# Performance work log

Hardware: AMD Instinct MI355X
Metric: run time of the kernel (lower is better)

The kernel has to match this reference:

```python
import jax, jax.numpy as jnp
import numpy as np

BN_EPS = 1e-5
K = 3  # number of nearest neighbors for interpolation


def setup_inputs() -> dict:
    key = jax.random.key(0)
    ks = jax.random.split(key, 16)
    B, N1, N2 = 8, 8192, 2048
    C2, C1, H = 256, 128, 256  # in_channels, skip_channels, out_channels
    total_in = C2 + C1
    inp = {
        "xyz1": jax.random.normal(ks[0], (B, 3, N1), dtype=jnp.float32),
        "xyz2": jax.random.normal(ks[1], (B, 3, N2), dtype=jnp.float32),
        "features1": jax.random.normal(ks[2], (B, C1, N1), dtype=jnp.float32),
        "features2": jax.random.normal(ks[3], (B, C2, N2), dtype=jnp.float32),
        # SharedMLP([total_in, H, H]): two 1x1 Conv1d + BatchNorm1d (eval mode) + ReLU
        "w1": jax.random.normal(ks[4], (H, total_in), dtype=jnp.float32) * 0.05,
        "b1": jax.random.normal(ks[5], (H,), dtype=jnp.float32) * 0.01,
        "g1": 1.0 + 0.1 * jax.random.normal(ks[6], (H,), dtype=jnp.float32),
        "be1": 0.1 * jax.random.normal(ks[7], (H,), dtype=jnp.float32),
        "m1": 0.1 * jax.random.normal(ks[8], (H,), dtype=jnp.float32),
        "v1": 0.5 + jax.random.uniform(ks[9], (H,), dtype=jnp.float32),
        "w2": jax.random.normal(ks[10], (H, H), dtype=jnp.float32) * 0.05,
        "b2": jax.random.normal(ks[11], (H,), dtype=jnp.float32) * 0.01,
        "g2": 1.0 + 0.1 * jax.random.normal(ks[12], (H,), dtype=jnp.float32),
        "be2": 0.1 * jax.random.normal(ks[13], (H,), dtype=jnp.float32),
        "m2": 0.1 * jax.random.normal(ks[14], (H,), dtype=jnp.float32),
        "v2": 0.5 + jax.random.uniform(ks[15], (H,), dtype=jnp.float32),
    }
    return inp


def _conv_bn_relu(x, w, b, g, be, m, v):
    # x: [B, Cin, N], w: [Cout, Cin] (1x1 conv), BN in eval mode
    y = jnp.einsum("oc,bcn->bon", w, x) + b[None, :, None]
    y = (y - m[None, :, None]) * (g / jnp.sqrt(v + BN_EPS))[None, :, None] + be[None, :, None]
    return jax.nn.relu(y)


def reference(xyz1, xyz2, features1, features2,
              w1, b1, g1, be1, m1, v1,
              w2, b2, g2, be2, m2, v2):
    # --- squared pairwise distances [B, N1, N2] ---
    x1 = jnp.transpose(xyz1, (0, 2, 1))  # [B, N1, 3]
    x2 = jnp.transpose(xyz2, (0, 2, 1))  # [B, N2, 3]
    sq = (jnp.sum(x1 * x1, axis=-1, keepdims=True)
          + jnp.sum(x2 * x2, axis=-1)[:, None, :]
          - 2.0 * jnp.einsum("bnd,bmd->bnm", x1, x2))
    # --- k=3 nearest neighbors (smallest sq distances) ---
    neg_d, idx = jax.lax.top_k(-sq, K)          # [B, N1, K]
    dist = jnp.maximum(-neg_d, 1e-10)
    weight = 1.0 / dist
    weight = weight / jnp.sum(weight, axis=-1, keepdims=True)  # [B, N1, K]
    # --- gather neighbor features and inverse-distance interpolate ---
    feat2_t = jnp.transpose(features2, (0, 2, 1))              # [B, N2, C2]
    neighbor = jax.vmap(lambda f, i: f[i])(feat2_t, idx)       # [B, N1, K, C2]
    interp = jnp.einsum("bnkc,bnk->bnc", neighbor, weight)     # [B, N1, C2]
    interp = jnp.transpose(interp, (0, 2, 1))                  # [B, C2, N1]
    # --- concat skip features and shared MLP ---
    x = jnp.concatenate([interp, features1], axis=1)           # [B, C2+C1, N1]
    x = _conv_bn_relu(x, w1, b1, g1, be1, m1, v1)
    x = _conv_bn_relu(x, w2, b2, g2, be2, m2, v2)
    return x
```

## Files before the change

### kernel.cpp

```cpp
#include <hip/hip_runtime.h>
#include <hip/hip_bf16.h>

typedef unsigned short u16;
typedef __attribute__((ext_vector_type(4))) float f32x4;
typedef __attribute__((ext_vector_type(8))) short short8;

#define BN_EPS 1e-5f

__device__ __forceinline__ u16 f2b(float x) {
  union { float f; unsigned int u; } v; v.f = x;
  unsigned int r = (v.u + 0x7FFFu + ((v.u >> 16) & 1u)) >> 16;
  return (u16)r;
}
__device__ __forceinline__ float b2f(u16 u) {
  union { unsigned int u; float f; } v; v.u = ((unsigned int)u) << 16;
  return v.f;
}

__global__ void prep_kernel(const float* __restrict__ w1, const float* __restrict__ b1,
                            const float* __restrict__ g1, const float* __restrict__ be1,
                            const float* __restrict__ m1, const float* __restrict__ v1,
                            const float* __restrict__ w2, const float* __restrict__ b2,
                            const float* __restrict__ g2, const float* __restrict__ be2,
                            const float* __restrict__ m2, const float* __restrict__ v2,
                            u16* __restrict__ w1b, u16* __restrict__ w2b,
                            float* __restrict__ al1, float* __restrict__ bt1,
                            float* __restrict__ al2, float* __restrict__ bt2) {
  int t = threadIdx.x;
  int blk = blockIdx.x;
  if (blk < 384) {
    int id = blk * 256 + t;
    unsigned o = (unsigned)id / 384u;
    unsigned c = (unsigned)id % 384u;
    w1b[(c >> 5) * 8192 + o * 32 + (c & 31)] = f2b(w1[id]);
  } else if (blk < 640) {
    int j = (blk - 384) * 256 + t;
    unsigned o = (unsigned)j >> 8;
    unsigned c = (unsigned)j & 255u;
    w2b[(c >> 5) * 8192 + o * 32 + (c & 31)] = f2b(w2[j]);
  } else if (blk == 640) {
    float a = g1[t] / sqrtf(v1[t] + BN_EPS);
    al1[t] = a;
    bt1[t] = (b1[t] - m1[t]) * a + be1[t];
  } else {
    float a = g2[t] / sqrtf(v2[t] + BN_EPS);
    al2[t] = a;
    bt2[t] = (b2[t] - m2[t]) * a + be2[t];
  }
}

__global__ void transpose_f2_kernel(const float* __restrict__ f2, u16* __restrict__ f2t) {
  __shared__ float tile[32][33];
  int t = threadIdx.x;
  int tx = t & 31, ty = t >> 5;
  int b = blockIdx.z;
  int n2t = blockIdx.x * 32, ct = blockIdx.y * 32;
#pragma unroll
  for (int i = 0; i < 4; ++i) {
    int c = ct + ty + i * 8;
    tile[ty + i * 8][tx] = f2[((size_t)b * 256 + c) * 2048 + n2t + tx];
  }
  __syncthreads();
#pragma unroll
  for (int i = 0; i < 4; ++i) {
    int n2 = n2t + ty + i * 8;
    f2t[((size_t)b * 2048 + n2) * 256 + ct + tx] = f2b(tile[tx][ty + i * 8]);
  }
}

__global__ __launch_bounds__(256) void knn_interp_kernel(
    const float* __restrict__ xyz1, const float* __restrict__ xyz2,
    const float* __restrict__ f1, const u16* __restrict__ f2t,
    u16* __restrict__ xb) {
  union Lds {
    struct { float4 pts[2048]; float md[256 * 3]; int mi[256 * 3]; } a;
    float f1t[128 * 65];
  };
  __shared__ Lds lds;
  __shared__ float wts[64 * 3];
  __shared__ int idxs[64 * 3];

  int t = threadIdx.x;
  int b = blockIdx.x >> 7;
  int n1_0 = (blockIdx.x & 127) * 64;
  int panel = blockIdx.x;

  const float* x2 = xyz2 + b * 3 * 2048;
  for (int j = t; j < 2048; j += 256) {
    float cx = x2[j], cy = x2[2048 + j], cz = x2[4096 + j];
    float nsq = (cx * cx + cy * cy) + cz * cz;
    lds.a.pts[j] = make_float4(cx, cy, cz, nsq);
  }
  __syncthreads();

  {
    int p = t & 63, s = t >> 6;
    int n1 = n1_0 + p;
    const float* x1 = xyz1 + b * 3 * 8192;
    float bx = x1[n1], by = x1[8192 + n1], bz = x1[16384 + n1];
    float n1sq = (bx * bx + by * by) + bz * bz;
    float nx = -2.f * bx, ny = -2.f * by, nz = -2.f * bz;
    float d0 = 3.4e38f, d1 = 3.4e38f, d2 = 3.4e38f;
    int i0 = 0, i1 = 0, i2 = 0;
    int jb = s * 512;
#pragma unroll 4
    for (int jj = 0; jj < 512; ++jj) {
      float4 c = lds.a.pts[jb + jj];
      float sq = fmaf(nx, c.x, fmaf(ny, c.y, fmaf(nz, c.z, n1sq + c.w)));
      int j = jb + jj;
      bool c0 = sq < d0, c1 = sq < d1, c2 = sq < d2;
      d2 = c1 ? d1 : (c2 ? sq : d2);  i2 = c1 ? i1 : (c2 ? j : i2);
      d1 = c0 ? d0 : (c1 ? sq : d1); i1 = c0 ? i0 : (c1 ? j : i1);
      d0 = c0 ? sq : d0;             i0 = c0 ? j : i0;
    }
    lds.a.md[t * 3 + 0] = d0; lds.a.md[t * 3 + 1] = d1; lds.a.md[t * 3 + 2] = d2;
    lds.a.mi[t * 3 + 0] = i0; lds.a.mi[t * 3 + 1] = i1; lds.a.mi[t * 3 + 2] = i2;
  }
  __syncthreads();
  if (t < 64) {
    float d0 = 3.4e38f, d1 = 3.4e38f, d2 = 3.4e38f;
    int i0 = 0, i1 = 0, i2 = 0;
#pragma unroll
    for (int s = 0; s < 4; ++s) {
#pragma unroll
      for (int k = 0; k < 3; ++k) {
        float d = lds.a.md[(s * 64 + t) * 3 + k];
        int i = lds.a.mi[(s * 64 + t) * 3 + k];
        bool c0 = d < d0, c1 = d < d1, c2 = d < d2;
        i2 = c1 ? i1 : (c2 ? i : i2);
        i1 = c0 ? i0 : (c1 ? i : i1);
        i0 = c0 ? i : i0;
        d2 = c1 ? d1 : (c2 ? d : d2);
        d1 = c0 ? d0 : (c1 ? d : d1);
        d0 = c0 ? d : d0;
      }
    }
    float e0 = fmaxf(d0, 1e-10f), e1 = fmaxf(d1, 1e-10f), e2 = fmaxf(d2, 1e-10f);
    float w0 = 1.0f / e0, w1 = 1.0f / e1, w2 = 1.0f / e2;
    float sm = (w0 + w1) + w2;
    wts[t * 3 + 0] = w0 / sm; wts[t * 3 + 1] = w1 / sm; wts[t * 3 + 2] = w2 / sm;
    idxs[t * 3 + 0] = i0 * 256; idxs[t * 3 + 1] = i1 * 256; idxs[t * 3 + 2] = i2 * 256;
  }
  __syncthreads();

  {
    const u16* f2tb = f2t + (size_t)b * 2048 * 256;
    size_t xbase = (size_t)panel * 24576 + (size_t)((t >> 5) * 2048) + (t & 31);
#pragma unroll 4
    for (int p = 0; p < 64; ++p) {
      int j0 = idxs[p * 3 + 0], j1 = idxs[p * 3 + 1], j2 = idxs[p * 3 + 2];
      float w0 = wts[p * 3 + 0], w1 = wts[p * 3 + 1], w2 = wts[p * 3 + 2];
      float v = (w0 * b2f(f2tb[j0 + t]) + w1 * b2f(f2tb[j1 + t]))
                + w2 * b2f(f2tb[j2 + t]);
      xb[xbase + p * 32] = f2b(v);
    }
  }
  __syncthreads();

  {
    const float* f1b = f1 + (size_t)b * 128 * 8192 + n1_0;
    for (int it = 0; it < 32; ++it) {
      int c = it * 4 + (t >> 6);
      int n = t & 63;
      lds.f1t[c * 65 + n] = f1b[(size_t)c * 8192 + n];
    }
    __syncthreads();
    for (int it = 0; it < 32; ++it) {
      int v = it * 256 + t;
      int c = v & 127, p = v >> 7;
      float val = lds.f1t[c * 65 + p];
      xb[(size_t)panel * 24576 + (size_t)(8 + (c >> 5)) * 2048 + p * 32 + (c & 31)] = f2b(val);
    }
  }
}

__global__ __launch_bounds__(256) void gemm_fused_kernel(
    const u16* __restrict__ xin, const u16* __restrict__ w1b,
    const u16* __restrict__ w2b,
    const float* __restrict__ al1, const float* __restrict__ bt1,
    const float* __restrict__ al2, const float* __restrict__ bt2,
    float* __restrict__ fout) {
  __shared__ u16 y1t[8 * 64 * 40];
  int t = threadIdx.x;
  int panel = blockIdx.x;
  int w = t >> 6, lane = t & 63, l15 = lane & 15, quad = lane >> 4;

  f32x4 acc[4][4];
#pragma unroll
  for (int m = 0; m < 4; ++m)
#pragma unroll
    for (int n = 0; n < 4; ++n)
      acc[m][n] = (f32x4){0.f, 0.f, 0.f, 0.f};

  {
    const u16* aw = w1b + (size_t)(w * 64 + l15) * 32 + quad * 8;
    const u16* bx = xin + (size_t)panel * (12 * 2048) + (size_t)l15 * 32 + quad * 8;
    short8 af[2][4], bf[2][4];
#pragma unroll
    for (int m = 0; m < 4; ++m)
      af[0][m] = *(const short8*)(aw + m * 512);
#pragma unroll
    for (int n = 0; n < 4; ++n)
      bf[0][n] = *(const short8*)(bx + n * 512);
#pragma unroll
    for (int kt = 0; kt < 12; ++kt) {
      int cur = kt & 1, nxt = cur ^ 1;
      if (kt < 11) {
#pragma unroll
        for (int m = 0; m < 4; ++m)
          af[nxt][m] = *(const short8*)(aw + (kt + 1) * 8192 + m * 512);
#pragma unroll
        for (int n = 0; n < 4; ++n)
          bf[nxt][n] = *(const short8*)(bx + (kt + 1) * 2048 + n * 512);
      }
#pragma unroll
      for (int m = 0; m < 4; ++m)
#pragma unroll
        for (int n = 0; n < 4; ++n)
          acc[m][n] = __builtin_amdgcn_mfma_f32_16x16x32_bf16(af[cur][m], bf[cur][n], acc[m][n], 0, 0, 0);
    }
  }

  {
    float al[4][4], bt[4][4];
#pragma unroll
    for (int m = 0; m < 4; ++m)
#pragma unroll
      for (int r = 0; r < 4; ++r) {
        int o = w * 64 + m * 16 + quad * 4 + r;
        al[m][r] = al1[o];
        bt[m][r] = bt1[o];
      }
#pragma unroll
    for (int m = 0; m < 4; ++m) {
      int kt2 = w * 2 + (m >> 1);
      int osub = (m & 1) * 16 + quad * 4;
#pragma unroll
      for (int n = 0; n < 4; ++n) {
        int col = n * 16 + l15;
        ushort4 pk;
        pk.x = f2b(fmaxf(fmaf(al[m][0], acc[m][n][0], bt[m][0]), 0.f));
        pk.y = f2b(fmaxf(fmaf(al[m][1], acc[m][n][1], bt[m][1]), 0.f));
        pk.z = f2b(fmaxf(fmaf(al[m][2], acc[m][n][2], bt[m][2]), 0.f));
        pk.w = f2b(fmaxf(fmaf(al[m][3], acc[m][n][3], bt[m][3]), 0.f));
        *(ushort4*)&y1t[(kt2 * 64 + col) * 40 + osub] = pk;
      }
    }
  }
  __syncthreads();

#pragma unroll
  for (int m = 0; m < 4; ++m)
#pragma unroll
    for (int n = 0; n < 4; ++n)
      acc[m][n] = (f32x4){0.f, 0.f, 0.f, 0.f};
  {
    const u16* aw = w2b + (size_t)(w * 64 + l15) * 32 + quad * 8;
    short8 af[2][4];
#pragma unroll
    for (int m = 0; m < 4; ++m)
      af[0][m] = *(const short8*)(aw + m * 512);
#pragma unroll
    for (int kt = 0; kt < 8; ++kt) {
      int cur = kt & 1, nxt = cur ^ 1;
      if (kt < 7) {
#pragma unroll
        for (int m = 0; m < 4; ++m)
          af[nxt][m] = *(const short8*)(aw + (kt + 1) * 8192 + m * 512);
      }
      short8 bf[4];
#pragma unroll
      for (int n = 0; n < 4; ++n)
        bf[n] = *(const short8*)&y1t[(kt * 64 + n * 16 + l15) * 40 + quad * 8];
#pragma unroll
      for (int m = 0; m < 4; ++m)
#pragma unroll
        for (int n = 0; n < 4; ++n)
          acc[m][n] = __builtin_amdgcn_mfma_f32_16x16x32_bf16(af[cur][m], bf[n], acc[m][n], 0, 0, 0);
    }
  }

  {
    float al[4][4], bt[4][4];
#pragma unroll
    for (int m = 0; m < 4; ++m)
#pragma unroll
      for (int r = 0; r < 4; ++r) {
        int o = w * 64 + m * 16 + quad * 4 + r;
        al[m][r] = al2[o];
        bt[m][r] = bt2[o];
      }
    int bb = panel >> 7;
    int n1base = (panel & 127) * 64;
#pragma unroll
    for (int m = 0; m < 4; ++m)
#pragma unroll
      for (int n = 0; n < 4; ++n) {
        int col = n * 16 + l15;
#pragma unroll
        for (int r = 0; r < 4; ++r) {
          int o = w * 64 + m * 16 + quad * 4 + r;
          float vv = fmaxf(fmaf(al[m][r], acc[m][n][r], bt[m][r]), 0.f);
          fout[(size_t)(bb * 256 + o) * 8192 + n1base + col] = vv;
        }
      }
  }
}

extern "C" void kernel_launch(void* const* d_in, const int* in_sizes, int n_in,
                              void* d_out, int out_size, void* d_ws, size_t ws_size,
                              hipStream_t stream) {
  const float* xyz1 = (const float*)d_in[0];
  const float* xyz2 = (const float*)d_in[1];
  const float* f1   = (const float*)d_in[2];
  const float* f2   = (const float*)d_in[3];
  const float* w1   = (const float*)d_in[4];
  const float* b1   = (const float*)d_in[5];
  const float* g1   = (const float*)d_in[6];
  const float* be1  = (const float*)d_in[7];
  const float* m1   = (const float*)d_in[8];
  const float* v1   = (const float*)d_in[9];
  const float* w2   = (const float*)d_in[10];
  const float* b2   = (const float*)d_in[11];
  const float* g2   = (const float*)d_in[12];
  const float* be2  = (const float*)d_in[13];
  const float* m2   = (const float*)d_in[14];
  const float* v2   = (const float*)d_in[15];

  char* ws = (char*)d_ws;
  u16* xb   = (u16*)(ws);
  u16* f2t  = (u16*)(ws + 50331648);
  u16* w1b  = (u16*)(ws + 83886080);
  u16* w2b  = (u16*)(ws + 84082688);
  float* al1 = (float*)(ws + 84213760);
  float* bt1 = (float*)(ws + 84214784);
  float* al2 = (float*)(ws + 84215808);
  float* bt2 = (float*)(ws + 84216832);
  float* out = (float*)d_out;

  prep_kernel<<<642, 256, 0, stream>>>(w1, b1, g1, be1, m1, v1,
                                       w2, b2, g2, be2, m2, v2,
                                       w1b, w2b, al1, bt1, al2, bt2);
  transpose_f2_kernel<<<dim3(64, 8, 8), 256, 0, stream>>>(f2, f2t);
  knn_interp_kernel<<<1024, 256, 0, stream>>>(xyz1, xyz2, f1, f2t, xb);
  gemm_fused_kernel<<<1024, 256, 0, stream>>>(xb, w1b, w2b, al1, bt1, al2, bt2, out);
}
```

Measured before the change: 233.5 us.

## Merge prep and transpose kernels, streamline kNN inner loop, vectorize gather

The weight-prep and feature-transpose kernels are merged into one launch to save a kernel launch. The kNN inner loop drops the per-query norm term, adding it back only after top-3 selection, and replaces the distance selects with med3/min instructions. The interpolation gather now loads and stores two bf16 channels per thread as 32-bit words, halving the memory instructions. Leaving out the query norm until after selection can change fp32 rounding near ties, which may pick a different neighbor.

```diff
diff --git a/kernel.cpp b/kernel.cpp
--- a/kernel.cpp
+++ b/kernel.cpp
@@ -16,29 +16,50 @@
   union { unsigned int u; float f; } v; v.u = ((unsigned int)u) << 16;
   return v.f;
 }
-
-__global__ void prep_kernel(const float* __restrict__ w1, const float* __restrict__ b1,
-                            const float* __restrict__ g1, const float* __restrict__ be1,
-                            const float* __restrict__ m1, const float* __restrict__ v1,
-                            const float* __restrict__ w2, const float* __restrict__ b2,
-                            const float* __restrict__ g2, const float* __restrict__ be2,
-                            const float* __restrict__ m2, const float* __restrict__ v2,
-                            u16* __restrict__ w1b, u16* __restrict__ w2b,
-                            float* __restrict__ al1, float* __restrict__ bt1,
-                            float* __restrict__ al2, float* __restrict__ bt2) {
+__device__ __forceinline__ float asf(unsigned u) {
+  union { unsigned u; float f; } v; v.u = u; return v.f;
+}
+
+__global__ void prep_transpose_kernel(
+    const float* __restrict__ f2, u16* __restrict__ f2t,
+    const float* __restrict__ w1, const float* __restrict__ b1,
+    const float* __restrict__ g1, const float* __restrict__ be1,
+    const float* __restrict__ m1, const float* __restrict__ v1,
+    const float* __restrict__ w2, const float* __restrict__ b2,
+    const float* __restrict__ g2, const float* __restrict__ be2,
+    const float* __restrict__ m2, const float* __restrict__ v2,
+    u16* __restrict__ w1b, u16* __restrict__ w2b,
+    float* __restrict__ al1, float* __restrict__ bt1,
+    float* __restrict__ al2, float* __restrict__ bt2) {
+  __shared__ float tile[32][33];
   int t = threadIdx.x;
   int blk = blockIdx.x;
-  if (blk < 384) {
-    int id = blk * 256 + t;
+  if (blk < 4096) {
+    int tx = t & 31, ty = t >> 5;
+    int b = (blk >> 9) & 7;
+    int n2t = (blk & 63) * 32, ct = ((blk >> 6) & 7) * 32;
+#pragma unroll
+    for (int i = 0; i < 4; ++i) {
+      int c = ct + ty + i * 8;
+      tile[ty + i * 8][tx] = f2[((size_t)b * 256 + c) * 2048 + n2t + tx];
+    }
+    __syncthreads();
+#pragma unroll
+    for (int i = 0; i < 4; ++i) {
+      int n2 = n2t + ty + i * 8;
+      f2t[((size_t)b * 2048 + n2) * 256 + ct + tx] = f2b(tile[tx][ty + i * 8]);
+    }
+  } else if (blk < 4480) {
+    int id = (blk - 4096) * 256 + t;
     unsigned o = (unsigned)id / 384u;
     unsigned c = (unsigned)id % 384u;
     w1b[(c >> 5) * 8192 + o * 32 + (c & 31)] = f2b(w1[id]);
-  } else if (blk < 640) {
-    int j = (blk - 384) * 256 + t;
+  } else if (blk < 4736) {
+    int j = (blk - 4480) * 256 + t;
     unsigned o = (unsigned)j >> 8;
     unsigned c = (unsigned)j & 255u;
     w2b[(c >> 5) * 8192 + o * 32 + (c & 31)] = f2b(w2[j]);
-  } else if (blk == 640) {
+  } else if (blk == 4736) {
     float a = g1[t] / sqrtf(v1[t] + BN_EPS);
     al1[t] = a;
     bt1[t] = (b1[t] - m1[t]) * a + be1[t];
@@ -46,25 +67,6 @@
     float a = g2[t] / sqrtf(v2[t] + BN_EPS);
     al2[t] = a;
     bt2[t] = (b2[t] - m2[t]) * a + be2[t];
-  }
-}
-
-__global__ void transpose_f2_kernel(const float* __restrict__ f2, u16* __restrict__ f2t) {
-  __shared__ float tile[32][33];
-  int t = threadIdx.x;
-  int tx = t & 31, ty = t >> 5;
-  int b = blockIdx.z;
-  int n2t = blockIdx.x * 32, ct = blockIdx.y * 32;
-#pragma unroll
-  for (int i = 0; i < 4; ++i) {
-    int c = ct + ty + i * 8;
-    tile[ty + i * 8][tx] = f2[((size_t)b * 256 + c) * 2048 + n2t + tx];
-  }
-  __syncthreads();
-#pragma unroll
-  for (int i = 0; i < 4; ++i) {
-    int n2 = n2t + ty + i * 8;
-    f2t[((size_t)b * 2048 + n2) * 256 + ct + tx] = f2b(tile[tx][ty + i * 8]);
   }
 }
 
@@ -93,12 +95,12 @@
   }
   __syncthreads();
 
+  const float* x1 = xyz1 + b * 3 * 8192;
+
   {
     int p = t & 63, s = t >> 6;
     int n1 = n1_0 + p;
-    const float* x1 = xyz1 + b * 3 * 8192;
     float bx = x1[n1], by = x1[8192 + n1], bz = x1[16384 + n1];
-    float n1sq = (bx * bx + by * by) + bz * bz;
     float nx = -2.f * bx, ny = -2.f * by, nz = -2.f * bz;
     float d0 = 3.4e38f, d1 = 3.4e38f, d2 = 3.4e38f;
     int i0 = 0, i1 = 0, i2 = 0;
@@ -106,12 +108,15 @@
 #pragma unroll 4
     for (int jj = 0; jj < 512; ++jj) {
       float4 c = lds.a.pts[jb + jj];
-      float sq = fmaf(nx, c.x, fmaf(ny, c.y, fmaf(nz, c.z, n1sq + c.w)));
+      float sq = fmaf(nx, c.x, fmaf(ny, c.y, fmaf(nz, c.z, c.w)));
       int j = jb + jj;
       bool c0 = sq < d0, c1 = sq < d1, c2 = sq < d2;
-      d2 = c1 ? d1 : (c2 ? sq : d2);  i2 = c1 ? i1 : (c2 ? j : i2);
-      d1 = c0 ? d0 : (c1 ? sq : d1); i1 = c0 ? i0 : (c1 ? j : i1);
-      d0 = c0 ? sq : d0;             i0 = c0 ? j : i0;
+      i2 = c1 ? i1 : (c2 ? j : i2);
+      i1 = c0 ? i0 : (c1 ? j : i1);
+      i0 = c0 ? j : i0;
+      d2 = __builtin_amdgcn_fmed3f(sq, d1, d2);
+      d1 = __builtin_amdgcn_fmed3f(sq, d0, d1);
+      d0 = fminf(sq, d0);
     }
     lds.a.md[t * 3 + 0] = d0; lds.a.md[t * 3 + 1] = d1; lds.a.md[t * 3 + 2] = d2;
     lds.a.mi[t * 3 + 0] = i0; lds.a.mi[t * 3 + 1] = i1; lds.a.mi[t * 3 + 2] = i2;
@@ -135,7 +140,10 @@
         d0 = c0 ? d : d0;
       }
     }
-    float e0 = fmaxf(d0, 1e-10f), e1 = fmaxf(d1, 1e-10f), e2 = fmaxf(d2, 1e-10f);
+    int n1 = n1_0 + t;
+    float bx = x1[n1], by = x1[8192 + n1], bz = x1[16384 + n1];
+    float nn = (bx * bx + by * by) + bz * bz;
+    float e0 = fmaxf(d0 + nn, 1e-10f), e1 = fmaxf(d1 + nn, 1e-10f), e2 = fmaxf(d2 + nn, 1e-10f);
     float w0 = 1.0f / e0, w1 = 1.0f / e1, w2 = 1.0f / e2;
     float sm = (w0 + w1) + w2;
     wts[t * 3 + 0] = w0 / sm; wts[t * 3 + 1] = w1 / sm; wts[t * 3 + 2] = w2 / sm;
@@ -145,14 +153,23 @@
 
   {
     const u16* f2tb = f2t + (size_t)b * 2048 * 256;
-    size_t xbase = (size_t)panel * 24576 + (size_t)((t >> 5) * 2048) + (t & 31);
+    int tc = t & 127;
+    int ph = t >> 7;
+    int ce = (2 * tc) & 31;
+    size_t xbase = (size_t)panel * 24576 + (size_t)(tc >> 4) * 2048 + ce;
 #pragma unroll 4
-    for (int p = 0; p < 64; ++p) {
+    for (int p2 = 0; p2 < 32; ++p2) {
+      int p = p2 * 2 + ph;
       int j0 = idxs[p * 3 + 0], j1 = idxs[p * 3 + 1], j2 = idxs[p * 3 + 2];
       float w0 = wts[p * 3 + 0], w1 = wts[p * 3 + 1], w2 = wts[p * 3 + 2];
-      float v = (w0 * b2f(f2tb[j0 + t]) + w1 * b2f(f2tb[j1 + t]))
-                + w2 * b2f(f2tb[j2 + t]);
-      xb[xbase + p * 32] = f2b(v);
+      unsigned a0 = *(const unsigned*)&f2tb[j0 + 2 * tc];
+      unsigned a1 = *(const unsigned*)&f2tb[j1 + 2 * tc];
+      unsigned a2 = *(const unsigned*)&f2tb[j2 + 2 * tc];
+      float vlo = (w0 * asf(a0 << 16) + w1 * asf(a1 << 16)) + w2 * asf(a2 << 16);
+      float vhi = (w0 * asf(a0 & 0xffff0000u) + w1 * asf(a1 & 0xffff0000u))
+                  + w2 * asf(a2 & 0xffff0000u);
+      unsigned pk = (unsigned)f2b(vlo) | ((unsigned)f2b(vhi) << 16);
+      *(unsigned*)&xb[xbase + (size_t)p * 32] = pk;
     }
   }
   __syncthreads();
@@ -338,10 +355,9 @@
   float* bt2 = (float*)(ws + 84216832);
   float* out = (float*)d_out;
 
-  prep_kernel<<<642, 256, 0, stream>>>(w1, b1, g1, be1, m1, v1,
-                                       w2, b2, g2, be2, m2, v2,
-                                       w1b, w2b, al1, bt1, al2, bt2);
-  transpose_f2_kernel<<<dim3(64, 8, 8), 256, 0, stream>>>(f2, f2t);
+  prep_transpose_kernel<<<4738, 256, 0, stream>>>(
+      f2, f2t, w1, b1, g1, be1, m1, v1, w2, b2, g2, be2, m2, v2,
+      w1b, w2b, al1, bt1, al2, bt2);
   knn_interp_kernel<<<1024, 256, 0, stream>>>(xyz1, xyz2, f1, f2t, xb);
   gemm_fused_kernel<<<1024, 256, 0, stream>>>(xb, w1b, w2b, al1, bt1, al2, bt2, out);
 }
```

Result: faster. 225.3 us (-3.5%).
